# Performance work log

Measured on AMD Instinct MI355X. Metric: run time of the kernel, lower is better.

## Reference

```python
import jax, jax.numpy as jnp
import numpy as np

N = 262144
D = 512
B = 1024  # number of segments/graphs (batch.max()+1 in the torch code)


def setup_inputs() -> dict:
    key = jax.random.key(0)
    k1, k2, k3, k4 = jax.random.split(key, 4)
    x = jax.random.normal(k1, (N, D), dtype=jnp.float32)
    batch = jnp.sort(jax.random.randint(k2, (N,), 0, B, dtype=jnp.int64))
    # score MLP params: Linear(D, D//4) -> Tanh -> Linear(D//4, 1)
    W1 = jax.random.normal(k3, (D, D // 4), dtype=jnp.float32) * (1.0 / np.sqrt(D))
    b1 = jnp.zeros((D // 4,), dtype=jnp.float32)
    W2 = jax.random.normal(k4, (D // 4, 1), dtype=jnp.float32) * (1.0 / np.sqrt(D // 4))
    b2 = jnp.zeros((1,), dtype=jnp.float32)
    return {"x": x, "batch": batch, "W1": W1, "b1": b1, "W2": W2, "b2": b2}


def reference(x, batch, W1, b1, W2, b2):
    # score MLP (dropout inactive at inference)
    scores = jnp.tanh(x @ W1 + b1) @ W2 + b2              # [N, 1]
    scores = scores - jnp.max(scores)                      # global max-shift for stability
    exp_s = jnp.exp(scores)                                # [N, 1]
    denom = jax.ops.segment_sum(exp_s, batch, num_segments=B)  # [B, 1]
    weight = exp_s / (denom[batch] + 1e-8)                 # [N, 1] segment softmax
    out = jax.ops.segment_sum(weight * x, batch, num_segments=B)  # [B, D]
    return out
```

## Files before the change

kernel.cpp:

```cpp
#include <hip/hip_runtime.h>
#include <hip/hip_bf16.h>

typedef _Float16 half8 __attribute__((ext_vector_type(8)));
typedef _Float16 half4v __attribute__((ext_vector_type(4)));
typedef float f32x4 __attribute__((ext_vector_type(4)));

#define BM 128
#define BK 64
#define LDK (BK + 8)

__global__ void prep_w1t(const float* __restrict__ W1, _Float16* __restrict__ W1T) {
    int idx = blockIdx.x * 256 + threadIdx.x;
    int n = idx >> 9;
    int k = idx & 511;
    W1T[idx] = (_Float16)W1[k * 128 + n];
}

__global__ __launch_bounds__(256) void score_kernel(
        const float* __restrict__ x, const _Float16* __restrict__ W1T,
        const float* __restrict__ b1, const float* __restrict__ W2,
        const float* __restrict__ b2, float* __restrict__ scores) {
    __shared__ _Float16 As[BM][LDK];
    __shared__ _Float16 Bs[128][LDK];
    const int tid = threadIdx.x;
    const int wave = tid >> 6, lane = tid & 63;
    const int quad = lane >> 4, col = lane & 15;
    const long row0 = (long)blockIdx.x * BM;

    f32x4 acc[2][8] = {};

    for (int kc = 0; kc < 512; kc += BK) {
        #pragma unroll
        for (int it = 0; it < 8; ++it) {
            int idx = it * 256 + tid;
            int r = idx >> 4, c4 = idx & 15;
            float4 v = *(const float4*)&x[(row0 + r) * 512 + kc + c4 * 4];
            half4v h; h[0] = (_Float16)v.x; h[1] = (_Float16)v.y;
                      h[2] = (_Float16)v.z; h[3] = (_Float16)v.w;
            *(half4v*)&As[r][c4 * 4] = h;
        }
        #pragma unroll
        for (int it = 0; it < 4; ++it) {
            int idx = it * 256 + tid;
            int n = idx >> 3, c8 = idx & 7;
            *(half8*)&Bs[n][c8 * 8] = *(const half8*)&W1T[n * 512 + kc + c8 * 8];
        }
        __syncthreads();
        #pragma unroll
        for (int ks = 0; ks < BK; ks += 32) {
            half8 a[2], bf[8];
            #pragma unroll
            for (int mt = 0; mt < 2; ++mt)
                a[mt] = *(half8*)&As[wave * 32 + mt * 16 + col][ks + quad * 8];
            #pragma unroll
            for (int nt = 0; nt < 8; ++nt)
                bf[nt] = *(half8*)&Bs[nt * 16 + col][ks + quad * 8];
            #pragma unroll
            for (int mt = 0; mt < 2; ++mt)
                #pragma unroll
                for (int nt = 0; nt < 8; ++nt)
                    acc[mt][nt] = __builtin_amdgcn_mfma_f32_16x16x32_f16(
                        a[mt], bf[nt], acc[mt][nt], 0, 0, 0);
        }
        __syncthreads();
    }

    float b1v[8], w2v[8];
    #pragma unroll
    for (int nt = 0; nt < 8; ++nt) {
        b1v[nt] = b1[nt * 16 + col];
        w2v[nt] = W2[nt * 16 + col];
    }
    float bias2 = b2[0];
    #pragma unroll
    for (int mt = 0; mt < 2; ++mt) {
        #pragma unroll
        for (int r = 0; r < 4; ++r) {
            float p = 0.f;
            #pragma unroll
            for (int nt = 0; nt < 8; ++nt)
                p += tanhf(acc[mt][nt][r] + b1v[nt]) * w2v[nt];
            #pragma unroll
            for (int off = 1; off < 16; off <<= 1) p += __shfl_xor(p, off);
            if (col == 0)
                scores[row0 + wave * 32 + mt * 16 + quad * 4 + r] = p + bias2;
        }
    }
}

__global__ void max_part(const float* __restrict__ scores, float* __restrict__ partial, int n) {
    __shared__ float red[256];
    int tid = threadIdx.x;
    float m = -1e30f;
    for (long i = (long)blockIdx.x * 256 + tid; i < n; i += (long)gridDim.x * 256)
        m = fmaxf(m, scores[i]);
    red[tid] = m; __syncthreads();
    for (int s = 128; s > 0; s >>= 1) {
        if (tid < s) red[tid] = fmaxf(red[tid], red[tid + s]);
        __syncthreads();
    }
    if (tid == 0) partial[blockIdx.x] = red[0];
}

__global__ void finalize_max(const float* __restrict__ partial, float* __restrict__ gmax,
                             float* __restrict__ denom, int nseg) {
    __shared__ float red[256];
    int tid = threadIdx.x;
    red[tid] = partial[tid]; __syncthreads();
    for (int s = 128; s > 0; s >>= 1) {
        if (tid < s) red[tid] = fmaxf(red[tid], red[tid + s]);
        __syncthreads();
    }
    if (tid == 0) gmax[0] = red[0];
    for (int b = tid; b < nseg; b += 256) denom[b] = 0.f;
}

__global__ void exp_denom(float* __restrict__ scores, const int* __restrict__ batch,
                          const float* __restrict__ gmax, float* __restrict__ denom, int n) {
    const int lane = threadIdx.x & 63;
    const float gm = gmax[0];
    for (long i = (long)blockIdx.x * blockDim.x + threadIdx.x; i < n;
         i += (long)gridDim.x * blockDim.x) {
        int seg = batch[i];
        float e = __expf(scores[i] - gm);
        scores[i] = e;
        float v = e;
        #pragma unroll
        for (int off = 1; off < 64; off <<= 1) {
            float ov = __shfl_down(v, off);
            int   os = __shfl_down(seg, off);
            if (lane + off < 64 && os == seg) v += ov;
        }
        int pseg = __shfl_up(seg, 1);
        if (lane == 0 || pseg != seg) atomicAdd(&denom[seg], v);
    }
}

__global__ void seg_starts(const int* __restrict__ batch, int* __restrict__ starts,
                           int n, int nseg) {
    for (long i = (long)blockIdx.x * blockDim.x + threadIdx.x; i < n;
         i += (long)gridDim.x * blockDim.x) {
        int s = batch[i];
        int p = (i == 0) ? -1 : batch[i - 1];
        for (int b = p + 1; b <= s; ++b) starts[b] = (int)i;
        if (i == n - 1)
            for (int b = s + 1; b <= nseg; ++b) starts[b] = n;
    }
}

__global__ __launch_bounds__(256) void pool_kernel(
        const float* __restrict__ x, const float* __restrict__ exps,
        const float* __restrict__ denom, const int* __restrict__ starts,
        float* __restrict__ out) {
    const int b = blockIdx.x;
    const int s0 = starts[b], s1 = starts[b + 1];
    const float dinv = 1.f / (denom[b] + 1e-8f);
    const int c = threadIdx.x * 2;
    float2 acc = make_float2(0.f, 0.f);
    for (int i = s0; i < s1; ++i) {
        float w = exps[i] * dinv;
        float2 xv = *(const float2*)&x[(long)i * 512 + c];
        acc.x += w * xv.x;
        acc.y += w * xv.y;
    }
    *(float2*)&out[(long)b * 512 + c] = acc;
}

extern "C" void kernel_launch(void* const* d_in, const int* in_sizes, int n_in,
                              void* d_out, int out_size, void* d_ws, size_t ws_size,
                              hipStream_t stream) {
    const float* x     = (const float*)d_in[0];
    const int*   batch = (const int*)d_in[1];
    const float* W1    = (const float*)d_in[2];
    const float* b1    = (const float*)d_in[3];
    const float* W2    = (const float*)d_in[4];
    const float* b2    = (const float*)d_in[5];
    float* out = (float*)d_out;

    const int N = in_sizes[1];
    const int D = 512;
    const int NSEG = out_size / D;

    _Float16* W1T   = (_Float16*)d_ws;
    float* scores   = (float*)((char*)d_ws + 131072);
    float* partial  = scores + N;
    float* gmax     = partial + 256;
    float* denom    = partial + 512;
    int*   starts   = (int*)(denom + NSEG);

    prep_w1t<<<256, 256, 0, stream>>>(W1, W1T);
    seg_starts<<<256, 256, 0, stream>>>(batch, starts, N, NSEG);
    score_kernel<<<N / BM, 256, 0, stream>>>(x, W1T, b1, W2, b2, scores);
    max_part<<<256, 256, 0, stream>>>(scores, partial, N);
    finalize_max<<<1, 256, 0, stream>>>(partial, gmax, denom, NSEG);
    exp_denom<<<256, 256, 0, stream>>>(scores, batch, gmax, denom, N);
    pool_kernel<<<NSEG, 256, 0, stream>>>(x, scores, denom, starts, out);
}
```

Baseline: 867.6 us.

## Fuse score, softmax and pooling into one persistent cooperative kernel

Replaces the chain of score, max, finalize, exp/denominator, segment-start and pooling kernels with one persistent kernel launched cooperatively. Grid-wide syncs separate the phases, and the global max is folded into the score epilogue. The GEMM tile shrinks to 64 rows so more blocks fit per CU. Pooling now uses float4 loads with two row-halves per block, removing several launches and the separate max pass over the scores, at the cost of grid barriers and a persistent grid of at most 1024 blocks.

```diff
diff --git a/kernel.cpp b/kernel.cpp
--- a/kernel.cpp
+++ b/kernel.cpp
@@ -1,13 +1,13 @@
 #include <hip/hip_runtime.h>
-#include <hip/hip_bf16.h>
+#include <hip/hip_cooperative_groups.h>
+
+namespace cg = cooperative_groups;
 
 typedef _Float16 half8 __attribute__((ext_vector_type(8)));
 typedef _Float16 half4v __attribute__((ext_vector_type(4)));
 typedef float f32x4 __attribute__((ext_vector_type(4)));
 
-#define BM 128
-#define BK 64
-#define LDK (BK + 8)
+#define LDK 72
 
 __global__ void prep_w1t(const float* __restrict__ W1, _Float16* __restrict__ W1T) {
     int idx = blockIdx.x * 256 + threadIdx.x;
@@ -16,54 +16,24 @@
     W1T[idx] = (_Float16)W1[k * 128 + n];
 }
 
-__global__ __launch_bounds__(256) void score_kernel(
-        const float* __restrict__ x, const _Float16* __restrict__ W1T,
-        const float* __restrict__ b1, const float* __restrict__ W2,
-        const float* __restrict__ b2, float* __restrict__ scores) {
-    __shared__ _Float16 As[BM][LDK];
-    __shared__ _Float16 Bs[128][LDK];
+__global__ __launch_bounds__(256, 4) void fused_kernel(
+        const float* __restrict__ x, const int* __restrict__ batch,
+        const _Float16* __restrict__ W1T, const float* __restrict__ b1,
+        const float* __restrict__ W2, const float* __restrict__ b2,
+        float* __restrict__ scores, float* __restrict__ partial,
+        float* __restrict__ denom, int* __restrict__ starts,
+        float* __restrict__ out, int N, int NSEG, int ntiles)
+{
+    __shared__ __align__(16) _Float16 As[64][LDK];
+    __shared__ __align__(16) _Float16 Bs[128][LDK];
+    __shared__ float red[256];
+
+    cg::grid_group gg = cg::this_grid();
     const int tid = threadIdx.x;
     const int wave = tid >> 6, lane = tid & 63;
     const int quad = lane >> 4, col = lane & 15;
-    const long row0 = (long)blockIdx.x * BM;
-
-    f32x4 acc[2][8] = {};
-
-    for (int kc = 0; kc < 512; kc += BK) {
-        #pragma unroll
-        for (int it = 0; it < 8; ++it) {
-            int idx = it * 256 + tid;
-            int r = idx >> 4, c4 = idx & 15;
-            float4 v = *(const float4*)&x[(row0 + r) * 512 + kc + c4 * 4];
-            half4v h; h[0] = (_Float16)v.x; h[1] = (_Float16)v.y;
-                      h[2] = (_Float16)v.z; h[3] = (_Float16)v.w;
-            *(half4v*)&As[r][c4 * 4] = h;
-        }
-        #pragma unroll
-        for (int it = 0; it < 4; ++it) {
-            int idx = it * 256 + tid;
-            int n = idx >> 3, c8 = idx & 7;
-            *(half8*)&Bs[n][c8 * 8] = *(const half8*)&W1T[n * 512 + kc + c8 * 8];
-        }
-        __syncthreads();
-        #pragma unroll
-        for (int ks = 0; ks < BK; ks += 32) {
-            half8 a[2], bf[8];
-            #pragma unroll
-            for (int mt = 0; mt < 2; ++mt)
-                a[mt] = *(half8*)&As[wave * 32 + mt * 16 + col][ks + quad * 8];
-            #pragma unroll
-            for (int nt = 0; nt < 8; ++nt)
-                bf[nt] = *(half8*)&Bs[nt * 16 + col][ks + quad * 8];
-            #pragma unroll
-            for (int mt = 0; mt < 2; ++mt)
-                #pragma unroll
-                for (int nt = 0; nt < 8; ++nt)
-                    acc[mt][nt] = __builtin_amdgcn_mfma_f32_16x16x32_f16(
-                        a[mt], bf[nt], acc[mt][nt], 0, 0, 0);
-        }
-        __syncthreads();
-    }
+    const long gsz = (long)gridDim.x * 256;
+    const long gtid = (long)blockIdx.x * 256 + tid;
 
     float b1v[8], w2v[8];
     #pragma unroll
@@ -71,56 +41,83 @@
         b1v[nt] = b1[nt * 16 + col];
         w2v[nt] = W2[nt * 16 + col];
     }
-    float bias2 = b2[0];
-    #pragma unroll
-    for (int mt = 0; mt < 2; ++mt) {
+    const float bias2 = b2[0];
+    float lmax = -1e30f;
+
+    for (int tile = blockIdx.x; tile < ntiles; tile += gridDim.x) {
+        const long row0 = (long)tile * 64;
+        f32x4 acc[8] = {};
+        for (int kc = 0; kc < 512; kc += 64) {
+            #pragma unroll
+            for (int it = 0; it < 4; ++it) {
+                int idx = it * 256 + tid;
+                int r = idx >> 4, c4 = idx & 15;
+                float4 v = *(const float4*)&x[(row0 + r) * 512 + kc + c4 * 4];
+                half4v h;
+                h[0] = (_Float16)v.x; h[1] = (_Float16)v.y;
+                h[2] = (_Float16)v.z; h[3] = (_Float16)v.w;
+                *(half4v*)&As[r][c4 * 4] = h;
+            }
+            #pragma unroll
+            for (int it = 0; it < 4; ++it) {
+                int idx = it * 256 + tid;
+                int n = idx >> 3, c8 = idx & 7;
+                *(half8*)&Bs[n][c8 * 8] = *(const half8*)&W1T[n * 512 + kc + c8 * 8];
+            }
+            __syncthreads();
+            #pragma unroll
+            for (int ks = 0; ks < 64; ks += 32) {
+                half8 a = *(half8*)&As[wave * 16 + col][ks + quad * 8];
+                half8 bf[8];
+                #pragma unroll
+                for (int nt = 0; nt < 8; ++nt)
+                    bf[nt] = *(half8*)&Bs[nt * 16 + col][ks + quad * 8];
+                #pragma unroll
+                for (int nt = 0; nt < 8; ++nt)
+                    acc[nt] = __builtin_amdgcn_mfma_f32_16x16x32_f16(a, bf[nt], acc[nt], 0, 0, 0);
+            }
+            __syncthreads();
+        }
         #pragma unroll
         for (int r = 0; r < 4; ++r) {
             float p = 0.f;
             #pragma unroll
             for (int nt = 0; nt < 8; ++nt)
-                p += tanhf(acc[mt][nt][r] + b1v[nt]) * w2v[nt];
+                p += tanhf(acc[nt][r] + b1v[nt]) * w2v[nt];
             #pragma unroll
             for (int off = 1; off < 16; off <<= 1) p += __shfl_xor(p, off);
-            if (col == 0)
-                scores[row0 + wave * 32 + mt * 16 + quad * 4 + r] = p + bias2;
+            p += bias2;
+            lmax = fmaxf(lmax, p);
+            if (col == 0) scores[row0 + wave * 16 + quad * 4 + r] = p;
         }
     }
-}
-
-__global__ void max_part(const float* __restrict__ scores, float* __restrict__ partial, int n) {
-    __shared__ float red[256];
-    int tid = threadIdx.x;
-    float m = -1e30f;
-    for (long i = (long)blockIdx.x * 256 + tid; i < n; i += (long)gridDim.x * 256)
-        m = fmaxf(m, scores[i]);
-    red[tid] = m; __syncthreads();
+    for (long i = gtid; i < N; i += gsz) {
+        int s = batch[i];
+        int pv = (i == 0) ? -1 : batch[i - 1];
+        for (int bb = pv + 1; bb <= s; ++bb) starts[bb] = (int)i;
+        if (i == N - 1)
+            for (int bb = s + 1; bb <= NSEG; ++bb) starts[bb] = N;
+    }
+    for (long bb = gtid; bb < NSEG; bb += gsz) denom[bb] = 0.f;
+    red[tid] = lmax;
+    __syncthreads();
     for (int s = 128; s > 0; s >>= 1) {
         if (tid < s) red[tid] = fmaxf(red[tid], red[tid + s]);
         __syncthreads();
     }
     if (tid == 0) partial[blockIdx.x] = red[0];
-}
+    gg.sync();
 
-__global__ void finalize_max(const float* __restrict__ partial, float* __restrict__ gmax,
-                             float* __restrict__ denom, int nseg) {
-    __shared__ float red[256];
-    int tid = threadIdx.x;
-    red[tid] = partial[tid]; __syncthreads();
+    float m = -1e30f;
+    for (int i = tid; i < (int)gridDim.x; i += 256) m = fmaxf(m, partial[i]);
+    red[tid] = m;
+    __syncthreads();
     for (int s = 128; s > 0; s >>= 1) {
         if (tid < s) red[tid] = fmaxf(red[tid], red[tid + s]);
         __syncthreads();
     }
-    if (tid == 0) gmax[0] = red[0];
-    for (int b = tid; b < nseg; b += 256) denom[b] = 0.f;
-}
-
-__global__ void exp_denom(float* __restrict__ scores, const int* __restrict__ batch,
-                          const float* __restrict__ gmax, float* __restrict__ denom, int n) {
-    const int lane = threadIdx.x & 63;
-    const float gm = gmax[0];
-    for (long i = (long)blockIdx.x * blockDim.x + threadIdx.x; i < n;
-         i += (long)gridDim.x * blockDim.x) {
+    const float gm = red[0];
+    for (long i = gtid; i < N; i += gsz) {
         int seg = batch[i];
         float e = __expf(scores[i] - gm);
         scores[i] = e;
@@ -128,42 +125,35 @@
         #pragma unroll
         for (int off = 1; off < 64; off <<= 1) {
             float ov = __shfl_down(v, off);
-            int   os = __shfl_down(seg, off);
+            int os = __shfl_down(seg, off);
             if (lane + off < 64 && os == seg) v += ov;
         }
         int pseg = __shfl_up(seg, 1);
         if (lane == 0 || pseg != seg) atomicAdd(&denom[seg], v);
     }
-}
+    gg.sync();
 
-__global__ void seg_starts(const int* __restrict__ batch, int* __restrict__ starts,
-                           int n, int nseg) {
-    for (long i = (long)blockIdx.x * blockDim.x + threadIdx.x; i < n;
-         i += (long)gridDim.x * blockDim.x) {
-        int s = batch[i];
-        int p = (i == 0) ? -1 : batch[i - 1];
-        for (int b = p + 1; b <= s; ++b) starts[b] = (int)i;
-        if (i == n - 1)
-            for (int b = s + 1; b <= nseg; ++b) starts[b] = n;
+    const int hh = tid >> 7;
+    const int c4 = (tid & 127) * 4;
+    float* comb = (float*)As;
+    for (int b = blockIdx.x; b < NSEG; b += gridDim.x) {
+        const int s0 = starts[b], s1 = starts[b + 1];
+        const float dinv = 1.f / (denom[b] + 1e-8f);
+        f32x4 acc = {};
+        for (int i = s0 + hh; i < s1; i += 2) {
+            float w = scores[i];
+            const f32x4 xv = *(const f32x4*)&x[(long)i * 512 + c4];
+            acc += w * xv;
+        }
+        __syncthreads();
+        if (hh) *(f32x4*)&comb[c4] = acc;
+        __syncthreads();
+        if (!hh) {
+            acc += *(f32x4*)&comb[c4];
+            acc *= dinv;
+            *(f32x4*)&out[(long)b * 512 + c4] = acc;
+        }
     }
-}
-
-__global__ __launch_bounds__(256) void pool_kernel(
-        const float* __restrict__ x, const float* __restrict__ exps,
-        const float* __restrict__ denom, const int* __restrict__ starts,
-        float* __restrict__ out) {
-    const int b = blockIdx.x;
-    const int s0 = starts[b], s1 = starts[b + 1];
-    const float dinv = 1.f / (denom[b] + 1e-8f);
-    const int c = threadIdx.x * 2;
-    float2 acc = make_float2(0.f, 0.f);
-    for (int i = s0; i < s1; ++i) {
-        float w = exps[i] * dinv;
-        float2 xv = *(const float2*)&x[(long)i * 512 + c];
-        acc.x += w * xv.x;
-        acc.y += w * xv.y;
-    }
-    *(float2*)&out[(long)b * 512 + c] = acc;
 }
 
 extern "C" void kernel_launch(void* const* d_in, const int* in_sizes, int n_in,
@@ -178,21 +168,27 @@
     float* out = (float*)d_out;
 
     const int N = in_sizes[1];
-    const int D = 512;
-    const int NSEG = out_size / D;
+    const int NSEG = out_size / 512;
+    const int ntiles = N / 64;
 
-    _Float16* W1T   = (_Float16*)d_ws;
-    float* scores   = (float*)((char*)d_ws + 131072);
-    float* partial  = scores + N;
-    float* gmax     = partial + 256;
-    float* denom    = partial + 512;
-    int*   starts   = (int*)(denom + NSEG);
+    _Float16* W1T  = (_Float16*)d_ws;
+    float* scores  = (float*)((char*)d_ws + 131072);
+    float* partial = scores + N;
+    float* denom   = partial + 1024;
+    int*   starts  = (int*)(denom + NSEG);
 
     prep_w1t<<<256, 256, 0, stream>>>(W1, W1T);
-    seg_starts<<<256, 256, 0, stream>>>(batch, starts, N, NSEG);
-    score_kernel<<<N / BM, 256, 0, stream>>>(x, W1T, b1, W2, b2, scores);
-    max_part<<<256, 256, 0, stream>>>(scores, partial, N);
-    finalize_max<<<1, 256, 0, stream>>>(partial, gmax, denom, NSEG);
-    exp_denom<<<256, 256, 0, stream>>>(scores, batch, gmax, denom, N);
-    pool_kernel<<<NSEG, 256, 0, stream>>>(x, scores, denom, starts, out);
+
+    int nb = 0;
+    if (hipOccupancyMaxActiveBlocksPerMultiprocessor(&nb, fused_kernel, 256, 0) != hipSuccess
+        || nb < 1)
+        nb = 4;
+    long grid = (long)nb * 256;
+    if (grid > 1024) grid = 1024;
+
+    void* args[] = { (void*)&x, (void*)&batch, (void*)&W1T, (void*)&b1, (void*)&W2, (void*)&b2,
+                     (void*)&scores, (void*)&partial, (void*)&denom, (void*)&starts,
+                     (void*)&out, (void*)&N, (void*)&NSEG, (void*)&ntiles };
+    hipLaunchCooperativeKernel((const void*)fused_kernel, dim3((int)grid), dim3(256),
+                               args, 0, stream);
 }
```

Result: slower. 1.003 ms (+15.6%).
